# Kernel optimization log

Hardware: AMD Instinct MI355X
Metric: run time of the kernel (lower is better)

The kernel has to match this reference:

```python
import jax, jax.numpy as jnp
import numpy as np

N = 2048   # nodes
E = 65536  # edges (avg degree 32)
F = 7      # node_feature_dim
S = 32     # state_dim
L = 16     # latent_dim
R = 3      # message passing rounds


def setup_inputs() -> dict:
    key = jax.random.key(0)
    ks = jax.random.split(key, 12)
    g = lambda k, shape, s: (jax.random.normal(k, shape, jnp.float32) * s)
    return dict(
        x=g(ks[0], (N, F), 1.0),
        edge_index=jax.random.randint(ks[1], (2, E), 0, N, dtype=jnp.int32),
        # input_net Linear(F->S)
        W_in=g(ks[2], (F, S), 0.3), b_in=jnp.zeros((S,), jnp.float32),
        # message nets: R x Linear(S->S)
        W_msg=g(ks[3], (R, S, S), 0.15), b_msg=jnp.zeros((R, S), jnp.float32),
        # GRU cells: R x (weight_ih, weight_hh) stored (in, 3*S) with torch gate order r,z,n
        W_ih=g(ks[4], (R, S, 3 * S), 0.15), W_hh=g(ks[5], (R, S, 3 * S), 0.15),
        b_ih=jnp.zeros((R, 3 * S), jnp.float32), b_hh=jnp.zeros((R, 3 * S), jnp.float32),
        # mu / logstd heads Linear(S->L)
        W_mu=g(ks[6], (S, L), 0.15), b_mu=jnp.zeros((L,), jnp.float32),
        W_ls=g(ks[7], (S, L), 0.15), b_ls=jnp.zeros((L,), jnp.float32),
        # decoder: Linear(2L->L), ReLU, Linear(L->1)
        W_d1=g(ks[8], (2 * L, L), 0.2), b_d1=jnp.zeros((L,), jnp.float32),
        W_d2=g(ks[9], (L, 1), 0.2), b_d2=jnp.zeros((1,), jnp.float32),
    )


def reference(x, edge_index, W_in, b_in, W_msg, b_msg, W_ih, W_hh, b_ih, b_hh,
              W_mu, b_mu, W_ls, b_ls, W_d1, b_d1, W_d2, b_d2):
    src, dst = edge_index[0], edge_index[1]
    # encoder
    state = jax.nn.relu(x @ W_in + b_in)  # [N, S]
    for r in range(R):
        message = jax.nn.relu(state @ W_msg[r] + b_msg[r])          # [N, S]
        aggregated = jax.ops.segment_sum(jnp.take(message, src, axis=0), dst,
                                         num_segments=N)            # [N, S]
        # GRUCell(aggregated, state), torch gate order: r, z, n
        gx = aggregated @ W_ih[r] + b_ih[r]                         # [N, 3S]
        gh = state @ W_hh[r] + b_hh[r]                              # [N, 3S]
        xr, xz, xn = jnp.split(gx, 3, axis=-1)
        hr, hz, hn = jnp.split(gh, 3, axis=-1)
        rg = jax.nn.sigmoid(xr + hr)
        zg = jax.nn.sigmoid(xz + hz)
        ng = jnp.tanh(xn + rg * hn)
        new_h = (1.0 - zg) * ng + zg * state
        state = state + new_h
    mu = state @ W_mu + b_mu        # [N, L]
    logstd = state @ W_ls + b_ls    # [N, L]
    # eval-mode reparameterize: z = mu
    z = mu
    # decode: Linear on concat([z_i, z_j]) == z_i @ W_d1[:L] + z_j @ W_d1[L:]
    a = z @ W_d1[:L]   # [N, L] contribution of row latent
    b = z @ W_d1[L:]   # [N, L] contribution of col latent
    h = jax.nn.relu(a[:, None, :] + b[None, :, :] + b_d1)  # [N, N, L]
    adj_logits = (h @ W_d2)[..., 0] + b_d2[0]              # [N, N]
    adj_logits = (adj_logits + adj_logits.T) / 2.0
    adj_recon = jax.nn.sigmoid(adj_logits)
    return (adj_recon, mu, logstd)
```

## Files before the change

### kernel.cpp

```cpp
#include <hip/hip_runtime.h>
#include <math.h>

#define NN 2048
#define EE 65536
#define FF 7
#define SS 32
#define LL 16
#define BKT 64
#define OCAP 4096
#define NBLK 256

struct Params {
    const float *x; const int *ei;
    const float *W_in, *b_in, *W_msg, *b_msg, *W_ih, *W_hh, *b_ih, *b_hh;
    const float *W_mu, *b_mu, *W_ls, *b_ls, *W_d1, *b_d1;
    float *st0, *st1, *st2, *msg0, *msg1, *msg2, *Abuf, *Bbuf;
    int *cnt, *ocnt, *olist, *bucket, *flags;
    float *out_mu, *out_ls;
};

__device__ __forceinline__ float fsig(float x) { return 1.f / (1.f + __expf(-x)); }
__device__ __forceinline__ float ftanh(float x) { return 1.f - 2.f / (__expf(2.f * x) + 1.f); }

__device__ __forceinline__ void stwt(float* p, float v) {
    __hip_atomic_store(p, v, __ATOMIC_RELAXED, __HIP_MEMORY_SCOPE_SYSTEM);
}
__device__ __forceinline__ void stwt_i(int* p, int v) {
    __hip_atomic_store(p, v, __ATOMIC_RELAXED, __HIP_MEMORY_SCOPE_SYSTEM);
}

__device__ __forceinline__ void gbar(int* flags, int phase) {
    __syncthreads();
    if (threadIdx.x == 0)
        __hip_atomic_store(flags + blockIdx.x, phase,
                           __ATOMIC_RELAXED, __HIP_MEMORY_SCOPE_SYSTEM);
    if (threadIdx.x < 64) {
        int l = threadIdx.x;
        for (;;) {
            int a = __hip_atomic_load(flags + l,       __ATOMIC_RELAXED, __HIP_MEMORY_SCOPE_SYSTEM);
            int b = __hip_atomic_load(flags + l + 64,  __ATOMIC_RELAXED, __HIP_MEMORY_SCOPE_SYSTEM);
            int c = __hip_atomic_load(flags + l + 128, __ATOMIC_RELAXED, __HIP_MEMORY_SCOPE_SYSTEM);
            int d = __hip_atomic_load(flags + l + 192, __ATOMIC_RELAXED, __HIP_MEMORY_SCOPE_SYSTEM);
            if (__all(a >= phase && b >= phase && c >= phase && d >= phase)) break;
            __builtin_amdgcn_s_sleep(1);
        }
    }
    __syncthreads();
}

__device__ __forceinline__ float gather_gru(int n, int s, int deg,
        const int* bucket, const int* ocnt, const int* olist,
        const float* msg_in, const float* st_in,
        const float* Wih, const float* Whh,
        const float* bih, const float* bhh) {
    const int* bk = bucket + n * BKT;
    int i0 = bk[s], i1 = bk[SS + s];
    float acc = 0.f;
#pragma unroll
    for (int k = 0; k < 32; k++) {
        int bsrc = __shfl(i0, k, 32);
        int src = (k < deg) ? bsrc : 0;
        float v = msg_in[src * SS + s];
        acc += (k < deg) ? v : 0.f;
    }
#pragma unroll
    for (int k = 0; k < 32; k++) {
        int kk = 32 + k;
        int bsrc = __shfl(i1, k, 32);
        int src = (kk < deg) ? bsrc : 0;
        float v = msg_in[src * SS + s];
        acc += (kk < deg) ? v : 0.f;
    }
    if (deg > BKT) {
        int oc = *ocnt; if (oc > OCAP) oc = OCAP;
        for (int i = 0; i < oc; i++)
            if (olist[2 * i + 1] == n) acc += msg_in[olist[2 * i] * SS + s];
    }
    float h0 = st_in[n * SS + s];
    float xr = bih[s], xz = bih[SS + s], xn = bih[2 * SS + s];
    float hr = bhh[s], hz = bhh[SS + s], hn = bhh[2 * SS + s];
#pragma unroll
    for (int k = 0; k < SS; k++) {
        float av = __shfl(acc, k, 32);
        float hv = __shfl(h0, k, 32);
        const float* wi = Wih + k * 3 * SS;
        const float* wh = Whh + k * 3 * SS;
        xr += av * wi[s];
        xz += av * wi[SS + s];
        xn += av * wi[2 * SS + s];
        hr += hv * wh[s];
        hz += hv * wh[SS + s];
        hn += hv * wh[2 * SS + s];
    }
    float rg = fsig(xr + hr);
    float zg = fsig(xz + hz);
    float ng = ftanh(xn + rg * hn);
    return h0 + (1.f - zg) * ng + zg * h0;
}

__global__ void __launch_bounds__(256) gnn(Params p) {
    int tid = threadIdx.x;
    int gid = blockIdx.x * 256 + tid;
    int n = gid >> 5, s = gid & 31;

    {
        int e = gid;
        int src = p.ei[e], dst = p.ei[EE + e];
        int slot = atomicAdd(&p.cnt[dst], 1);
        if (slot < BKT) stwt_i(&p.bucket[dst * BKT + slot], src);
        else {
            int oi = atomicAdd(p.ocnt, 1);
            if (oi < OCAP) { stwt_i(&p.olist[2 * oi], src); stwt_i(&p.olist[2 * oi + 1], dst); }
        }
        const float* xr = p.x + n * FF;
        float acc = p.b_in[s];
#pragma unroll
        for (int k = 0; k < FF; k++) acc += xr[k] * p.W_in[k * SS + s];
        float st = fmaxf(acc, 0.f);
        p.st0[n * SS + s] = st;
        float m = p.b_msg[s];
#pragma unroll
        for (int k = 0; k < SS; k++) m += __shfl(st, k, 32) * p.W_msg[k * SS + s];
        stwt(&p.msg0[n * SS + s], fmaxf(m, 0.f));
    }
    gbar(p.flags, 1);

    int deg = p.cnt[n];

    {
        float st = gather_gru(n, s, deg, p.bucket, p.ocnt, p.olist, p.msg0, p.st0,
                              p.W_ih, p.W_hh, p.b_ih, p.b_hh);
        p.st1[n * SS + s] = st;
        const float* Wm = p.W_msg + 1 * SS * SS;
        const float* bm = p.b_msg + 1 * SS;
        float mv = bm[s];
#pragma unroll
        for (int k = 0; k < SS; k++) mv += __shfl(st, k, 32) * Wm[k * SS + s];
        stwt(&p.msg1[n * SS + s], fmaxf(mv, 0.f));
    }
    gbar(p.flags, 2);

    {
        float st = gather_gru(n, s, deg, p.bucket, p.ocnt, p.olist, p.msg1, p.st1,
                              p.W_ih + SS * 3 * SS, p.W_hh + SS * 3 * SS,
                              p.b_ih + 3 * SS, p.b_hh + 3 * SS);
        p.st2[n * SS + s] = st;
        const float* Wm = p.W_msg + 2 * SS * SS;
        const float* bm = p.b_msg + 2 * SS;
        float mv = bm[s];
#pragma unroll
        for (int k = 0; k < SS; k++) mv += __shfl(st, k, 32) * Wm[k * SS + s];
        stwt(&p.msg2[n * SS + s], fmaxf(mv, 0.f));
    }
    gbar(p.flags, 3);

    {
        float st = gather_gru(n, s, deg, p.bucket, p.ocnt, p.olist, p.msg2, p.st2,
                              p.W_ih + 2 * SS * 3 * SS, p.W_hh + 2 * SS * 3 * SS,
                              p.b_ih + 2 * 3 * SS, p.b_hh + 2 * 3 * SS);
        int l = s & 15;
        const float* W = (s < 16) ? p.W_mu : p.W_ls;
        float v = (s < 16) ? p.b_mu[l] : p.b_ls[l];
#pragma unroll
        for (int k = 0; k < SS; k++) v += __shfl(st, k, 32) * W[k * LL + l];
        if (s < 16) p.out_mu[n * LL + l] = v; else p.out_ls[n * LL + l] = v;
        const float* Wd = p.W_d1 + ((s < 16) ? 0 : LL * LL);
        float ab = (s < 16) ? p.b_d1[l] : 0.f;
#pragma unroll
        for (int k = 0; k < LL; k++) ab += __shfl(v, k, 32) * Wd[k * LL + l];
        if (s < 16) p.Abuf[n * LL + l] = ab; else p.Bbuf[n * LL + l] = ab;
    }
}

__global__ __launch_bounds__(256) void dec_kernel(const float* __restrict__ Abuf,
                                                  const float* __restrict__ Bbuf,
                                                  const float* __restrict__ W_d2,
                                                  const float* __restrict__ b_d2,
                                                  float* __restrict__ out) {
    __shared__ float ldsAj[LL * 64];
    __shared__ float ldsBj[LL * 64];
    __shared__ float ldsT[64 * 65];
    int t = blockIdx.x;
    int bi = (int)((65.f - sqrtf(4225.f - 8.f * (float)t)) * 0.5f);
    if (bi < 0) bi = 0;
    if (bi > 31) bi = 31;
    while (bi > 0 && (65 * bi - bi * bi) / 2 > t) bi--;
    while (bi < 31 && (65 * (bi + 1) - (bi + 1) * (bi + 1)) / 2 <= t) bi++;
    int bj = bi + (t - (65 * bi - bi * bi) / 2);
    int i0 = bi * 64, j0 = bj * 64;
    int tid = threadIdx.x;

    {
        int jr = tid >> 2, q = tid & 3;
        float4 va = ((const float4*)(Abuf + (size_t)(j0 + jr) * LL))[q];
        float4 vb = ((const float4*)(Bbuf + (size_t)(j0 + jr) * LL))[q];
        int l4 = q * 4;
        ldsAj[(l4 + 0) * 64 + jr] = va.x; ldsAj[(l4 + 1) * 64 + jr] = va.y;
        ldsAj[(l4 + 2) * 64 + jr] = va.z; ldsAj[(l4 + 3) * 64 + jr] = va.w;
        ldsBj[(l4 + 0) * 64 + jr] = vb.x; ldsBj[(l4 + 1) * 64 + jr] = vb.y;
        ldsBj[(l4 + 2) * 64 + jr] = vb.z; ldsBj[(l4 + 3) * 64 + jr] = vb.w;
    }
    __syncthreads();

    int jo = tid & 63;
    int ig = tid >> 6;
    float aj[LL], bjr[LL], w[LL];
#pragma unroll
    for (int l = 0; l < LL; l++) {
        aj[l] = ldsAj[l * 64 + jo];
        bjr[l] = ldsBj[l * 64 + jo];
        w[l] = W_d2[l];
    }
    float bd2 = b_d2[0];
    int j = j0 + jo;

#pragma unroll 2
    for (int ii = 0; ii < 16; ii++) {
        int i = i0 + ig * 16 + ii;
        const float4* Ai4 = (const float4*)(Abuf + (size_t)i * LL);
        const float4* Bi4 = (const float4*)(Bbuf + (size_t)i * LL);
        float4 a0 = Ai4[0], a1 = Ai4[1], a2 = Ai4[2], a3 = Ai4[3];
        float4 b0 = Bi4[0], b1 = Bi4[1], b2 = Bi4[2], b3 = Bi4[3];
        float ai[LL] = {a0.x, a0.y, a0.z, a0.w, a1.x, a1.y, a1.z, a1.w,
                        a2.x, a2.y, a2.z, a2.w, a3.x, a3.y, a3.z, a3.w};
        float bi_[LL] = {b0.x, b0.y, b0.z, b0.w, b1.x, b1.y, b1.z, b1.w,
                         b2.x, b2.y, b2.z, b2.w, b3.x, b3.y, b3.z, b3.w};
        float accij = 0.f, accji = 0.f;
#pragma unroll
        for (int l = 0; l < LL; l++) {
            accij += w[l] * fmaxf(ai[l] + bjr[l], 0.f);
            accji += w[l] * fmaxf(aj[l] + bi_[l], 0.f);
        }
        float logit = 0.5f * (accij + accji) + bd2;
        float p = 1.f / (1.f + __expf(-logit));
        out[(size_t)i * NN + j] = p;
        ldsT[jo * 65 + ig * 16 + ii] = p;
    }

    if (bi != bj) {
        __syncthreads();
        int jj = tid >> 2, qi = tid & 3;
        float v[16];
#pragma unroll
        for (int m = 0; m < 16; m++) v[m] = ldsT[jj * 65 + qi * 16 + m];
        float4* dst = (float4*)(out + (size_t)(j0 + jj) * NN + i0 + qi * 16);
#pragma unroll
        for (int q4 = 0; q4 < 4; q4++)
            dst[q4] = make_float4(v[4 * q4], v[4 * q4 + 1], v[4 * q4 + 2], v[4 * q4 + 3]);
    }
}

extern "C" void kernel_launch(void* const* d_in, const int* in_sizes, int n_in,
                              void* d_out, int out_size, void* d_ws, size_t ws_size,
                              hipStream_t stream) {
    Params p;
    p.x     = (const float*)d_in[0];
    p.ei    = (const int*)d_in[1];
    p.W_in  = (const float*)d_in[2];
    p.b_in  = (const float*)d_in[3];
    p.W_msg = (const float*)d_in[4];
    p.b_msg = (const float*)d_in[5];
    p.W_ih  = (const float*)d_in[6];
    p.W_hh  = (const float*)d_in[7];
    p.b_ih  = (const float*)d_in[8];
    p.b_hh  = (const float*)d_in[9];
    p.W_mu  = (const float*)d_in[10];
    p.b_mu  = (const float*)d_in[11];
    p.W_ls  = (const float*)d_in[12];
    p.b_ls  = (const float*)d_in[13];
    p.W_d1  = (const float*)d_in[14];
    p.b_d1  = (const float*)d_in[15];
    const float* W_d2 = (const float*)d_in[16];
    const float* b_d2 = (const float*)d_in[17];

    float* ws = (float*)d_ws;
    p.st0  = ws;
    p.st1  = p.st0 + NN * SS;
    p.st2  = p.st1 + NN * SS;
    p.msg0 = p.st2 + NN * SS;
    p.msg1 = p.msg0 + NN * SS;
    p.msg2 = p.msg1 + NN * SS;
    p.Abuf = p.msg2 + NN * SS;
    p.Bbuf = p.Abuf + NN * LL;
    p.cnt  = (int*)(p.Bbuf + NN * LL);
    p.ocnt = p.cnt + NN;
    p.flags = p.ocnt + 1;
    p.olist = p.flags + NBLK;
    p.bucket = p.olist + 2 * OCAP;

    float* out_adj = (float*)d_out;
    p.out_mu  = out_adj + (size_t)NN * NN;
    p.out_ls  = p.out_mu + NN * LL;

    hipMemsetAsync(p.cnt, 0, (NN + 1 + NBLK) * sizeof(int), stream);

    gnn<<<NBLK, 256, 0, stream>>>(p);

    dec_kernel<<<528, 256, 0, stream>>>(p.Abuf, p.Bbuf, W_d2, b_d2, out_adj);
}
```

Before: 68.57 us.

## Use master-block grid barrier and keep GRU state in registers

The grid barrier changes from every block polling all 256 flags to block 0 polling the flags and then publishing a single go flag that the other blocks spin on. The per-node state now stays in registers across rounds instead of being written to and reread from st0/st1/st2 global buffers. Bucket indices are loaded once rather than once per round. This cuts polling traffic and global memory round trips, but adds an extra hop of latency through block 0 at each barrier.

```diff
diff --git a/kernel.cpp b/kernel.cpp
--- a/kernel.cpp
+++ b/kernel.cpp
@@ -14,8 +14,8 @@
     const float *x; const int *ei;
     const float *W_in, *b_in, *W_msg, *b_msg, *W_ih, *W_hh, *b_ih, *b_hh;
     const float *W_mu, *b_mu, *W_ls, *b_ls, *W_d1, *b_d1;
-    float *st0, *st1, *st2, *msg0, *msg1, *msg2, *Abuf, *Bbuf;
-    int *cnt, *ocnt, *olist, *bucket, *flags;
+    float *msg0, *msg1, *msg2, *Abuf, *Bbuf;
+    int *cnt, *ocnt, *olist, *bucket, *flags, *go;
     float *out_mu, *out_ls;
 };
 
@@ -28,33 +28,40 @@
 __device__ __forceinline__ void stwt_i(int* p, int v) {
     __hip_atomic_store(p, v, __ATOMIC_RELAXED, __HIP_MEMORY_SCOPE_SYSTEM);
 }
-
-__device__ __forceinline__ void gbar(int* flags, int phase) {
+__device__ __forceinline__ int ldsys(const int* p) {
+    return __hip_atomic_load(p, __ATOMIC_RELAXED, __HIP_MEMORY_SCOPE_SYSTEM);
+}
+
+__device__ __forceinline__ void gbar(int* flags, int* go, int phase) {
     __syncthreads();
-    if (threadIdx.x == 0)
-        __hip_atomic_store(flags + blockIdx.x, phase,
-                           __ATOMIC_RELAXED, __HIP_MEMORY_SCOPE_SYSTEM);
-    if (threadIdx.x < 64) {
-        int l = threadIdx.x;
-        for (;;) {
-            int a = __hip_atomic_load(flags + l,       __ATOMIC_RELAXED, __HIP_MEMORY_SCOPE_SYSTEM);
-            int b = __hip_atomic_load(flags + l + 64,  __ATOMIC_RELAXED, __HIP_MEMORY_SCOPE_SYSTEM);
-            int c = __hip_atomic_load(flags + l + 128, __ATOMIC_RELAXED, __HIP_MEMORY_SCOPE_SYSTEM);
-            int d = __hip_atomic_load(flags + l + 192, __ATOMIC_RELAXED, __HIP_MEMORY_SCOPE_SYSTEM);
-            if (__all(a >= phase && b >= phase && c >= phase && d >= phase)) break;
-            __builtin_amdgcn_s_sleep(1);
+    if (blockIdx.x == 0) {
+        if (threadIdx.x < 64) {
+            if (threadIdx.x == 0)
+                stwt_i(flags + 0, phase);
+            int l = threadIdx.x;
+            for (;;) {
+                int a = ldsys(flags + l);
+                int b = ldsys(flags + l + 64);
+                int c = ldsys(flags + l + 128);
+                int d = ldsys(flags + l + 192);
+                if (__all(a >= phase && b >= phase && c >= phase && d >= phase)) break;
+                __builtin_amdgcn_s_sleep(2);
+            }
+            if (threadIdx.x == 0)
+                stwt_i(go, phase);
         }
+    } else if (threadIdx.x == 0) {
+        stwt_i(flags + blockIdx.x, phase);
+        while (ldsys(go) < phase) __builtin_amdgcn_s_sleep(8);
     }
     __syncthreads();
 }
 
-__device__ __forceinline__ float gather_gru(int n, int s, int deg,
-        const int* bucket, const int* ocnt, const int* olist,
-        const float* msg_in, const float* st_in,
+__device__ __forceinline__ float gather_gru(int s, int deg, int i0, int i1,
+        const int* ocnt, const int* olist, int n,
+        const float* msg_in, float h0,
         const float* Wih, const float* Whh,
         const float* bih, const float* bhh) {
-    const int* bk = bucket + n * BKT;
-    int i0 = bk[s], i1 = bk[SS + s];
     float acc = 0.f;
 #pragma unroll
     for (int k = 0; k < 32; k++) {
@@ -76,7 +83,6 @@
         for (int i = 0; i < oc; i++)
             if (olist[2 * i + 1] == n) acc += msg_in[olist[2 * i] * SS + s];
     }
-    float h0 = st_in[n * SS + s];
     float xr = bih[s], xz = bih[SS + s], xn = bih[2 * SS + s];
     float hr = bhh[s], hz = bhh[SS + s], hn = bhh[2 * SS + s];
 #pragma unroll
@@ -103,6 +109,8 @@
     int gid = blockIdx.x * 256 + tid;
     int n = gid >> 5, s = gid & 31;
 
+    float stc;
+
     {
         int e = gid;
         int src = p.ei[e], dst = p.ei[EE + e];
@@ -116,53 +124,52 @@
         float acc = p.b_in[s];
 #pragma unroll
         for (int k = 0; k < FF; k++) acc += xr[k] * p.W_in[k * SS + s];
-        float st = fmaxf(acc, 0.f);
-        p.st0[n * SS + s] = st;
+        stc = fmaxf(acc, 0.f);
         float m = p.b_msg[s];
 #pragma unroll
-        for (int k = 0; k < SS; k++) m += __shfl(st, k, 32) * p.W_msg[k * SS + s];
+        for (int k = 0; k < SS; k++) m += __shfl(stc, k, 32) * p.W_msg[k * SS + s];
         stwt(&p.msg0[n * SS + s], fmaxf(m, 0.f));
     }
-    gbar(p.flags, 1);
+    gbar(p.flags, p.go, 1);
 
     int deg = p.cnt[n];
-
-    {
-        float st = gather_gru(n, s, deg, p.bucket, p.ocnt, p.olist, p.msg0, p.st0,
-                              p.W_ih, p.W_hh, p.b_ih, p.b_hh);
-        p.st1[n * SS + s] = st;
+    int i0 = p.bucket[n * BKT + s];
+    int i1 = p.bucket[n * BKT + SS + s];
+
+    {
+        stc = gather_gru(s, deg, i0, i1, p.ocnt, p.olist, n, p.msg0, stc,
+                         p.W_ih, p.W_hh, p.b_ih, p.b_hh);
         const float* Wm = p.W_msg + 1 * SS * SS;
         const float* bm = p.b_msg + 1 * SS;
         float mv = bm[s];
 #pragma unroll
-        for (int k = 0; k < SS; k++) mv += __shfl(st, k, 32) * Wm[k * SS + s];
+        for (int k = 0; k < SS; k++) mv += __shfl(stc, k, 32) * Wm[k * SS + s];
         stwt(&p.msg1[n * SS + s], fmaxf(mv, 0.f));
     }
-    gbar(p.flags, 2);
-
-    {
-        float st = gather_gru(n, s, deg, p.bucket, p.ocnt, p.olist, p.msg1, p.st1,
-                              p.W_ih + SS * 3 * SS, p.W_hh + SS * 3 * SS,
-                              p.b_ih + 3 * SS, p.b_hh + 3 * SS);
-        p.st2[n * SS + s] = st;
+    gbar(p.flags, p.go, 2);
+
+    {
+        stc = gather_gru(s, deg, i0, i1, p.ocnt, p.olist, n, p.msg1, stc,
+                         p.W_ih + SS * 3 * SS, p.W_hh + SS * 3 * SS,
+                         p.b_ih + 3 * SS, p.b_hh + 3 * SS);
         const float* Wm = p.W_msg + 2 * SS * SS;
         const float* bm = p.b_msg + 2 * SS;
         float mv = bm[s];
 #pragma unroll
-        for (int k = 0; k < SS; k++) mv += __shfl(st, k, 32) * Wm[k * SS + s];
+        for (int k = 0; k < SS; k++) mv += __shfl(stc, k, 32) * Wm[k * SS + s];
         stwt(&p.msg2[n * SS + s], fmaxf(mv, 0.f));
     }
-    gbar(p.flags, 3);
-
-    {
-        float st = gather_gru(n, s, deg, p.bucket, p.ocnt, p.olist, p.msg2, p.st2,
-                              p.W_ih + 2 * SS * 3 * SS, p.W_hh + 2 * SS * 3 * SS,
-                              p.b_ih + 2 * 3 * SS, p.b_hh + 2 * 3 * SS);
+    gbar(p.flags, p.go, 3);
+
+    {
+        stc = gather_gru(s, deg, i0, i1, p.ocnt, p.olist, n, p.msg2, stc,
+                         p.W_ih + 2 * SS * 3 * SS, p.W_hh + 2 * SS * 3 * SS,
+                         p.b_ih + 2 * 3 * SS, p.b_hh + 2 * 3 * SS);
         int l = s & 15;
         const float* W = (s < 16) ? p.W_mu : p.W_ls;
         float v = (s < 16) ? p.b_mu[l] : p.b_ls[l];
 #pragma unroll
-        for (int k = 0; k < SS; k++) v += __shfl(st, k, 32) * W[k * LL + l];
+        for (int k = 0; k < SS; k++) v += __shfl(stc, k, 32) * W[k * LL + l];
         if (s < 16) p.out_mu[n * LL + l] = v; else p.out_ls[n * LL + l] = v;
         const float* Wd = p.W_d1 + ((s < 16) ? 0 : LL * LL);
         float ab = (s < 16) ? p.b_d1[l] : 0.f;
@@ -274,10 +281,7 @@
     const float* b_d2 = (const float*)d_in[17];
 
     float* ws = (float*)d_ws;
-    p.st0  = ws;
-    p.st1  = p.st0 + NN * SS;
-    p.st2  = p.st1 + NN * SS;
-    p.msg0 = p.st2 + NN * SS;
+    p.msg0 = ws;
     p.msg1 = p.msg0 + NN * SS;
     p.msg2 = p.msg1 + NN * SS;
     p.Abuf = p.msg2 + NN * SS;
@@ -285,14 +289,15 @@
     p.cnt  = (int*)(p.Bbuf + NN * LL);
     p.ocnt = p.cnt + NN;
     p.flags = p.ocnt + 1;
-    p.olist = p.flags + NBLK;
+    p.go   = p.flags + NBLK;
+    p.olist = p.go + 4;
     p.bucket = p.olist + 2 * OCAP;
 
     float* out_adj = (float*)d_out;
     p.out_mu  = out_adj + (size_t)NN * NN;
     p.out_ls  = p.out_mu + NN * LL;
 
-    hipMemsetAsync(p.cnt, 0, (NN + 1 + NBLK) * sizeof(int), stream);
+    hipMemsetAsync(p.cnt, 0, (NN + 1 + NBLK + 4) * sizeof(int), stream);
 
     gnn<<<NBLK, 256, 0, stream>>>(p);
 
```

Result: faster. 60.17 us (-12.3%).
